# Kernel optimization log

Hardware: AMD Instinct MI355X
Metric: run time of the kernel (lower is better)

## Reference

```python
import math
import jax, jax.numpy as jnp
import numpy as np

B, T, D = 32, 2048, 512
FACTOR = 2
TOP_K = int(FACTOR * math.log(T))  # = 15, static (T is static under jit)


def setup_inputs() -> dict:
    key = jax.random.key(0)
    ks = jax.random.split(key, 11)
    s = 1.0 / math.sqrt(D)
    return {
        "query": jax.random.normal(ks[0], (B, T, D), jnp.float32),
        "key_in": jax.random.normal(ks[1], (B, T, D), jnp.float32),
        "value": jax.random.normal(ks[2], (B, T, D), jnp.float32),
        "Wq": jax.random.normal(ks[3], (D, D), jnp.float32) * s,
        "bq": jnp.zeros((D,), jnp.float32),
        "Wk": jax.random.normal(ks[4], (D, D), jnp.float32) * s,
        "bk": jnp.zeros((D,), jnp.float32),
        "Wv": jax.random.normal(ks[5], (D, D), jnp.float32) * s,
        "bv": jnp.zeros((D,), jnp.float32),
        "Wo": jax.random.normal(ks[6], (D, D), jnp.float32) * s,
        "bo": jnp.zeros((D,), jnp.float32),
    }


def reference(query, key_in, value, Wq, bq, Wk, bk, Wv, bv, Wo, bo):
    # Linear projections (query/key/value lengths are equal here, so no trimming)
    q = query @ Wq + bq      # [B, T, D]
    k = key_in @ Wk + bk     # [B, T, D]
    v = value @ Wv + bv      # [B, T, D]

    # FFT cross-correlation along the time axis
    qf = jnp.fft.rfft(q, axis=1)
    kf = jnp.fft.rfft(k, axis=1)
    attn_weights = jnp.fft.irfft(qf * jnp.conj(kf), n=T, axis=1)  # [B, T, D]

    # Top-k delay selection on the feature-mean autocorrelation
    autocorr_mean = attn_weights.mean(axis=-1)           # [B, T]
    _, topk_delays = jax.lax.top_k(autocorr_mean, TOP_K)  # [B, K] int32

    # Sum of circularly-rolled values over the top-k delays.
    # tf.roll(v, s, 0): out[t] = v[(t - s) mod T]; accumulate via scan over K
    def body(acc, d):  # d: [B] delays for this k
        rolled = jax.vmap(lambda vb, db: jnp.roll(vb, db, axis=0))(v, d)
        return acc + rolled, None

    rolled_sum, _ = jax.lax.scan(body, jnp.zeros_like(v), topk_delays.T)  # [B, T, D]

    # Softmax over the feature axis (independent of k in the original loop)
    soft_attn = jax.nn.softmax(attn_weights, axis=-1)    # [B, T, D]
    attn_output = rolled_sum * soft_attn                 # [B, T, D]

    return attn_output @ Wo + bo
```

## Files before the change

kernel.cpp:

```cpp
#include <hip/hip_runtime.h>

#define NFFT 2048
#define LDK 40
#define FFT_PAD(p) ((p) + ((p) >> 5))

typedef __attribute__((ext_vector_type(8))) short bf16x8;
typedef __attribute__((ext_vector_type(4))) float f32x4;

__device__ __forceinline__ unsigned short f2bf_rne(float x) {
  unsigned u = __float_as_uint(x);
  return (unsigned short)((u + 0x7fffu + ((u >> 16) & 1u)) >> 16);
}
__device__ __forceinline__ float bf2f(unsigned short h) {
  return __uint_as_float(((unsigned)h) << 16);
}

__device__ __forceinline__ void gemm_decode(int lin, int& n0, int& b,
                                            int& t0) {
  const int xcd = lin & 7;
  const int j = lin >> 3;
  const int nblk = j & 3;
  const int y = (j >> 2) * 8 + xcd;
  n0 = nblk * 128;
  b = y >> 4;
  t0 = (y & 15) * 128;
}

__global__ __launch_bounds__(256) void wsplit_kernel(
    const float* __restrict__ W0, const float* __restrict__ W1,
    const float* __restrict__ W2, const float* __restrict__ W3,
    unsigned short* __restrict__ out) {
  __shared__ float tile[32][33];
  const float* W = (blockIdx.z == 0) ? W0
                   : (blockIdx.z == 1) ? W1
                   : (blockIdx.z == 2) ? W2 : W3;
  unsigned short* hi = out + (size_t)blockIdx.z * 524288;
  unsigned short* lo = hi + 262144;
  const int k0 = blockIdx.x * 32, n0 = blockIdx.y * 32;
  const int c = threadIdx.x & 31, r = threadIdx.x >> 5;
#pragma unroll
  for (int p = 0; p < 4; p++)
    tile[r + 8 * p][c] = W[(size_t)(k0 + r + 8 * p) * 512 + n0 + c];
  __syncthreads();
#pragma unroll
  for (int p = 0; p < 4; p++) {
    int nn = r + 8 * p;
    float x = tile[c][nn];
    unsigned u = __float_as_uint(x);
    unsigned short h = (unsigned short)(u >> 16);
    float hf = __uint_as_float(u & 0xffff0000u);
    unsigned short l = f2bf_rne(x - hf);
    hi[(size_t)(n0 + nn) * 512 + k0 + c] = h;
    lo[(size_t)(n0 + nn) * 512 + k0 + c] = l;
  }
}

__global__ __launch_bounds__(256) void proj_gemm_split(
    const float* __restrict__ X, const unsigned short* __restrict__ WThi,
    const unsigned short* __restrict__ WTlo, const float* __restrict__ bias,
    float* __restrict__ YT) {
  __shared__ __align__(16) unsigned short Wh[128 * LDK];
  __shared__ __align__(16) unsigned short Wl[128 * LDK];
  __shared__ __align__(16) unsigned short Xh[128 * LDK];
  __shared__ __align__(16) unsigned short Xl[128 * LDK];
  const int tid = threadIdx.x;
  int n0, b, t0;
  gemm_decode(blockIdx.x, n0, b, t0);
  const int w = tid >> 6, l = tid & 63;
  const int wn = (w & 1) * 64;
  const int wt = (w >> 1) * 64;
  const int fr = l & 15;
  const int fk = (l >> 4) * 8;

  f32x4 acc[4][4];
#pragma unroll
  for (int i = 0; i < 4; i++)
#pragma unroll
    for (int j = 0; j < 4; j++) acc[i][j] = (f32x4)0.f;

  const int srow = tid >> 1, scol = (tid & 1) * 16;
  const float* Xg = X + ((size_t)(b * 2048 + t0 + srow)) * 512 + scol;
  const unsigned short* Whg = WThi + ((size_t)(n0 + srow)) * 512 + scol;
  const unsigned short* Wlg = WTlo + ((size_t)(n0 + srow)) * 512 + scol;
  unsigned short* XhL = &Xh[srow * LDK + scol];
  unsigned short* XlL = &Xl[srow * LDK + scol];
  unsigned short* WhL = &Wh[srow * LDK + scol];
  unsigned short* WlL = &Wl[srow * LDK + scol];

  float xv[16];
  uint4 wh0, wh1, wl0, wl1;
  *(float4*)&xv[0] = *(const float4*)&Xg[0];
  *(float4*)&xv[4] = *(const float4*)&Xg[4];
  *(float4*)&xv[8] = *(const float4*)&Xg[8];
  *(float4*)&xv[12] = *(const float4*)&Xg[12];
  wh0 = *(const uint4*)&Whg[0];
  wh1 = *(const uint4*)&Whg[8];
  wl0 = *(const uint4*)&Wlg[0];
  wl1 = *(const uint4*)&Wlg[8];

  for (int k0 = 0; k0 < 512; k0 += 32) {
    union { unsigned short us[16]; uint4 q[2]; } hb, lb;
#pragma unroll
    for (int i = 0; i < 16; i++) {
      unsigned u = __float_as_uint(xv[i]);
      hb.us[i] = (unsigned short)(u >> 16);
      float hf = __uint_as_float(u & 0xffff0000u);
      lb.us[i] = f2bf_rne(xv[i] - hf);
    }
    __syncthreads();
    *(uint4*)&XhL[0] = hb.q[0];
    *(uint4*)&XhL[8] = hb.q[1];
    *(uint4*)&XlL[0] = lb.q[0];
    *(uint4*)&XlL[8] = lb.q[1];
    *(uint4*)&WhL[0] = wh0;
    *(uint4*)&WhL[8] = wh1;
    *(uint4*)&WlL[0] = wl0;
    *(uint4*)&WlL[8] = wl1;
    __syncthreads();
    const int k1 = k0 + 32;
    if (k1 < 512) {
      *(float4*)&xv[0] = *(const float4*)&Xg[k1];
      *(float4*)&xv[4] = *(const float4*)&Xg[k1 + 4];
      *(float4*)&xv[8] = *(const float4*)&Xg[k1 + 8];
      *(float4*)&xv[12] = *(const float4*)&Xg[k1 + 12];
      wh0 = *(const uint4*)&Whg[k1];
      wh1 = *(const uint4*)&Whg[k1 + 8];
      wl0 = *(const uint4*)&Wlg[k1];
      wl1 = *(const uint4*)&Wlg[k1 + 8];
    }
    bf16x8 ah[4], al[4], bh[4], bl[4];
#pragma unroll
    for (int i = 0; i < 4; i++) {
      ah[i] = *(const bf16x8*)&Wh[(wn + 16 * i + fr) * LDK + fk];
      al[i] = *(const bf16x8*)&Wl[(wn + 16 * i + fr) * LDK + fk];
      bh[i] = *(const bf16x8*)&Xh[(wt + 16 * i + fr) * LDK + fk];
      bl[i] = *(const bf16x8*)&Xl[(wt + 16 * i + fr) * LDK + fk];
    }
#pragma unroll
    for (int i = 0; i < 4; i++)
#pragma unroll
      for (int j = 0; j < 4; j++) {
        acc[i][j] = __builtin_amdgcn_mfma_f32_16x16x32_bf16(ah[i], bh[j],
                                                            acc[i][j], 0, 0, 0);
        acc[i][j] = __builtin_amdgcn_mfma_f32_16x16x32_bf16(al[i], bh[j],
                                                            acc[i][j], 0, 0, 0);
        acc[i][j] = __builtin_amdgcn_mfma_f32_16x16x32_bf16(ah[i], bl[j],
                                                            acc[i][j], 0, 0, 0);
      }
  }
  const size_t obase = (size_t)b * 512 * 2048;
#pragma unroll
  for (int i = 0; i < 4; i++) {
#pragma unroll
    for (int r = 0; r < 4; r++) {
      int n = n0 + wn + 16 * i + (l >> 4) * 4 + r;
      float bsc = bias[n];
      size_t row = obase + (size_t)n * 2048 + t0 + wt + (l & 15);
#pragma unroll
      for (int j = 0; j < 4; j++) YT[row + 16 * j] = acc[i][j][r] + bsc;
    }
  }
}

__global__ __launch_bounds__(256) void gemm_bf16_vproj(
    const float* __restrict__ X, const unsigned short* __restrict__ WThi,
    const float* __restrict__ bias, unsigned short* __restrict__ Vbf) {
  __shared__ __align__(16) unsigned short Ws[128 * LDK];
  __shared__ __align__(16) unsigned short Xs[128 * LDK];
  const int tid = threadIdx.x;
  int n0, b, t0;
  gemm_decode(blockIdx.x, n0, b, t0);
  const int w = tid >> 6, l = tid & 63;
  const int wr = (w & 1) * 64;
  const int wc = (w >> 1) * 64;
  const int fr = l & 15, fk = (l >> 4) * 8;

  f32x4 acc[4][4];
#pragma unroll
  for (int i = 0; i < 4; i++)
#pragma unroll
    for (int j = 0; j < 4; j++) acc[i][j] = (f32x4)0.f;

  const int srow = tid >> 1, scol = (tid & 1) * 16;
  const float* Xg = X + ((size_t)(b * 2048 + t0 + srow)) * 512 + scol;
  const unsigned short* Wg = WThi + ((size_t)(n0 + srow)) * 512 + scol;
  unsigned short* XsL = &Xs[srow * LDK + scol];
  unsigned short* WsL = &Ws[srow * LDK + scol];

  float xv[16];
  uint4 w0, w1;
  *(float4*)&xv[0] = *(const float4*)&Xg[0];
  *(float4*)&xv[4] = *(const float4*)&Xg[4];
  *(float4*)&xv[8] = *(const float4*)&Xg[8];
  *(float4*)&xv[12] = *(const float4*)&Xg[12];
  w0 = *(const uint4*)&Wg[0];
  w1 = *(const uint4*)&Wg[8];

  for (int k0 = 0; k0 < 512; k0 += 32) {
    union { unsigned short us[16]; uint4 q[2]; } hb;
#pragma unroll
    for (int i = 0; i < 16; i++) hb.us[i] = f2bf_rne(xv[i]);
    __syncthreads();
    *(uint4*)&XsL[0] = hb.q[0];
    *(uint4*)&XsL[8] = hb.q[1];
    *(uint4*)&WsL[0] = w0;
    *(uint4*)&WsL[8] = w1;
    __syncthreads();
    const int k1 = k0 + 32;
    if (k1 < 512) {
      *(float4*)&xv[0] = *(const float4*)&Xg[k1];
      *(float4*)&xv[4] = *(const float4*)&Xg[k1 + 4];
      *(float4*)&xv[8] = *(const float4*)&Xg[k1 + 8];
      *(float4*)&xv[12] = *(const float4*)&Xg[k1 + 12];
      w0 = *(const uint4*)&Wg[k1];
      w1 = *(const uint4*)&Wg[k1 + 8];
    }
    bf16x8 af[4], bf[4];
#pragma unroll
    for (int i = 0; i < 4; i++) {
      af[i] = *(const bf16x8*)&Xs[(wr + 16 * i + fr) * LDK + fk];
      bf[i] = *(const bf16x8*)&Ws[(wc + 16 * i + fr) * LDK + fk];
    }
#pragma unroll
    for (int i = 0; i < 4; i++)
#pragma unroll
      for (int j = 0; j < 4; j++)
        acc[i][j] = __builtin_amdgcn_mfma_f32_16x16x32_bf16(af[i], bf[j],
                                                            acc[i][j], 0, 0, 0);
  }
  float bj[4];
#pragma unroll
  for (int j = 0; j < 4; j++) bj[j] = bias[n0 + wc + 16 * j + (l & 15)];
#pragma unroll
  for (int i = 0; i < 4; i++) {
#pragma unroll
    for (int r = 0; r < 4; r++) {
      int t = t0 + wr + 16 * i + (l >> 4) * 4 + r;
      unsigned short* vrow = Vbf + ((size_t)(b * 2048 + t)) * 512;
#pragma unroll
      for (int j = 0; j < 4; j++) {
        int d = n0 + wc + 16 * j + (l & 15);
        vrow[d] = f2bf_rne(acc[i][j][r] + bj[j]);
      }
    }
  }
}

__global__ __launch_bounds__(256) void gemm_bf16_out(
    const unsigned short* __restrict__ Abf,
    const unsigned short* __restrict__ WThi, const float* __restrict__ bias,
    float* __restrict__ Y) {
  __shared__ __align__(16) unsigned short Ws[128 * LDK];
  __shared__ __align__(16) unsigned short Xs[128 * LDK];
  const int tid = threadIdx.x;
  int n0, b, t0;
  gemm_decode(blockIdx.x, n0, b, t0);
  const int w = tid >> 6, l = tid & 63;
  const int wr = (w & 1) * 64;
  const int wc = (w >> 1) * 64;
  const int fr = l & 15, fk = (l >> 4) * 8;

  f32x4 acc[4][4];
#pragma unroll
  for (int i = 0; i < 4; i++)
#pragma unroll
    for (int j = 0; j < 4; j++) acc[i][j] = (f32x4)0.f;

  const int srow = tid >> 1, scol = (tid & 1) * 16;
  const unsigned short* Ag = Abf + ((size_t)(b * 2048 + t0 + srow)) * 512 + scol;
  const unsigned short* Wg = WThi + ((size_t)(n0 + srow)) * 512 + scol;
  unsigned short* XsL = &Xs[srow * LDK + scol];
  unsigned short* WsL = &Ws[srow * LDK + scol];

  uint4 a0, a1, w0, w1;
  a0 = *(const uint4*)&Ag[0];
  a1 = *(const uint4*)&Ag[8];
  w0 = *(const uint4*)&Wg[0];
  w1 = *(const uint4*)&Wg[8];

  for (int k0 = 0; k0 < 512; k0 += 32) {
    __syncthreads();
    *(uint4*)&XsL[0] = a0;
    *(uint4*)&XsL[8] = a1;
    *(uint4*)&WsL[0] = w0;
    *(uint4*)&WsL[8] = w1;
    __syncthreads();
    const int k1 = k0 + 32;
    if (k1 < 512) {
      a0 = *(const uint4*)&Ag[k1];
      a1 = *(const uint4*)&Ag[k1 + 8];
      w0 = *(const uint4*)&Wg[k1];
      w1 = *(const uint4*)&Wg[k1 + 8];
    }
    bf16x8 af[4], bf[4];
#pragma unroll
    for (int i = 0; i < 4; i++) {
      af[i] = *(const bf16x8*)&Xs[(wr + 16 * i + fr) * LDK + fk];
      bf[i] = *(const bf16x8*)&Ws[(wc + 16 * i + fr) * LDK + fk];
    }
#pragma unroll
    for (int i = 0; i < 4; i++)
#pragma unroll
      for (int j = 0; j < 4; j++)
        acc[i][j] = __builtin_amdgcn_mfma_f32_16x16x32_bf16(af[i], bf[j],
                                                            acc[i][j], 0, 0, 0);
  }
  float bj[4];
#pragma unroll
  for (int j = 0; j < 4; j++) bj[j] = bias[n0 + wc + 16 * j + (l & 15)];
#pragma unroll
  for (int i = 0; i < 4; i++) {
#pragma unroll
    for (int r = 0; r < 4; r++) {
      int t = t0 + wr + 16 * i + (l >> 4) * 4 + r;
      float* yrow = Y + ((size_t)(b * 2048 + t)) * 512;
#pragma unroll
      for (int j = 0; j < 4; j++) {
        int n = n0 + wc + 16 * j + (l & 15);
        yrow[n] = acc[i][j][r] + bj[j];
      }
    }
  }
}

__device__ __forceinline__ float2 cadd(float2 a, float2 b) {
  return make_float2(a.x + b.x, a.y + b.y);
}
__device__ __forceinline__ float2 csub(float2 a, float2 b) {
  return make_float2(a.x - b.x, a.y - b.y);
}
__device__ __forceinline__ float2 cmulf(float2 a, float2 b) {
  return make_float2(a.x * b.x - a.y * b.y, a.x * b.y + a.y * b.x);
}
template <int SGN>
__device__ __forceinline__ float2 mul_i(float2 a) {
  return (SGN < 0) ? make_float2(a.y, -a.x) : make_float2(-a.y, a.x);
}

template <int SGN>
__device__ __forceinline__ void dft4(float2 v[4]) {
  float2 b0 = cadd(v[0], v[2]);
  float2 b2 = csub(v[0], v[2]);
  float2 b1 = cadd(v[1], v[3]);
  float2 b3 = mul_i<SGN>(csub(v[1], v[3]));
  v[0] = cadd(b0, b1);
  v[2] = csub(b0, b1);
  v[1] = cadd(b2, b3);
  v[3] = csub(b2, b3);
}

template <int SGN>
__device__ __forceinline__ void dft8(float2 v[8]) {
  const float C = 0.70710678118654752f;
  float2 e[4], o[4];
#pragma unroll
  for (int i = 0; i < 4; i++) {
    e[i] = cadd(v[i], v[i + 4]);
    o[i] = csub(v[i], v[i + 4]);
  }
  {
    float s = o[1].x, t = o[1].y;
    o[1] = (SGN < 0) ? make_float2(C * (s + t), C * (t - s))
                     : make_float2(C * (s - t), C * (s + t));
  }
  o[2] = mul_i<SGN>(o[2]);
  {
    float s = o[3].x, t = o[3].y;
    o[3] = (SGN < 0) ? make_float2(C * (t - s), -C * (s + t))
                     : make_float2(-C * (s + t), C * (s - t));
  }
  dft4<SGN>(e);
  dft4<SGN>(o);
  v[0] = e[0]; v[2] = e[1]; v[4] = e[2]; v[6] = e[3];
  v[1] = o[0]; v[3] = o[1]; v[5] = o[2]; v[7] = o[3];
}

__device__ __forceinline__ void twiddle8_pair(float2 vz[8], float2 vw[8],
                                              float ang) {
  float2 T;
  __sincosf(ang, &T.y, &T.x);
  float2 t = T;
  vz[1] = cmulf(vz[1], t);
  vw[1] = cmulf(vw[1], t);
#pragma unroll
  for (int r = 2; r < 8; r++) {
    t = cmulf(t, T);
    vz[r] = cmulf(vz[r], t);
    vw[r] = cmulf(vw[r], t);
  }
}
__device__ __forceinline__ void twiddle8_one(float2 v[8], float ang) {
  float2 T;
  __sincosf(ang, &T.y, &T.x);
  float2 t = T;
  v[1] = cmulf(v[1], t);
#pragma unroll
  for (int r = 2; r < 8; r++) {
    t = cmulf(t, T);
    v[r] = cmulf(v[r], t);
  }
}

__global__ __launch_bounds__(256) void fft_correlate(
    float* __restrict__ qT, const float* __restrict__ kT) {
  __shared__ float2 ldsZ[2112];
  __shared__ float2 ldsW[2112];
  const int b = blockIdx.x;
  const int d0 = blockIdx.y * 2;
  const int tid = threadIdx.x;
  const size_t base = ((size_t)b * 512 + d0) * 2048;

  const float W1 = -6.28318530717958647692f / 2048.f;
  const int j2 = tid & 31, j3 = tid & 3;
  const int s1 = tid >> 5, s2 = tid >> 2;
  const int f1 = ((tid & 7) << 6) | (tid & 56) | (tid >> 6);
  const int pt = tid + (tid >> 5);
  const int b2 = 264 * s1 + j2;
  const int b3 = 33 * s2 + j3;

  float2 vz[8], vw[8];
#pragma unroll
  for (int r = 0; r < 8; r++) {
    int t = tid + (r << 8);
    vz[r] = make_float2(qT[base + t], qT[base + 2048 + t]);
    vw[r] = make_float2(kT[base + t], kT[base + 2048 + t]);
  }

  dft8<-1>(vz);
  dft8<-1>(vw);
  twiddle8_pair(vz, vw, W1 * (float)tid);
#pragma unroll
  for (int r = 0; r < 8; r++) {
    ldsZ[pt + 264 * r] = vz[r];
    ldsW[pt + 264 * r] = vw[r];
  }
  __syncthreads();
#pragma unroll
  for (int m = 0; m < 8; m++) {
    vz[m] = ldsZ[b2 + 33 * m];
    vw[m] = ldsW[b2 + 33 * m];
  }
  dft8<-1>(vz);
  dft8<-1>(vw);
  twiddle8_pair(vz, vw, (W1 * 8.f) * (float)j2);
#pragma unroll
  for (int r = 0; r < 8; r++) {
    ldsZ[b2 + 33 * r] = vz[r];
    ldsW[b2 + 33 * r] = vw[r];
  }
  __syncthreads();
#pragma unroll
  for (int m = 0; m < 8; m++) {
    vz[m] = ldsZ[b3 + 4 * m];
    vw[m] = ldsW[b3 + 4 * m];
  }
  dft8<-1>(vz);
  dft8<-1>(vw);
  twiddle8_pair(vz, vw, (W1 * 64.f) * (float)j3);
#pragma unroll
  for (int r = 0; r < 8; r++) {
    ldsZ[b3 + 4 * r] = vz[r];
    ldsW[b3 + 4 * r] = vw[r];
  }
  __syncthreads();
  {
    float2 za[4], zb[4], wa[4], wb[4];
    const int pb = f1 << 2;
#pragma unroll
    for (int c = 0; c < 4; c++) {
      za[c] = ldsZ[FFT_PAD(pb + c)];
      zb[c] = ldsZ[FFT_PAD(pb + 16 + c)];
      wa[c] = ldsW[FFT_PAD(pb + c)];
      wb[c] = ldsW[FFT_PAD(pb + 16 + c)];
    }
    dft4<-1>(za);
    dft4<-1>(zb);
    dft4<-1>(wa);
    dft4<-1>(wb);
    __syncthreads();
#pragma unroll
    for (int c = 0; c < 4; c++) {
      ldsZ[pt + 528 * c] = za[c];
      ldsZ[pt + 264 + 528 * c] = zb[c];
      ldsW[pt + 528 * c] = wa[c];
      ldsW[pt + 264 + 528 * c] = wb[c];
    }
  }
  __syncthreads();

  float2 G[8];
#pragma unroll
  for (int r = 0; r < 8; r++) {
    int f = tid + (r << 8);
    int fn = (NFFT - f) & (NFFT - 1);
    float2 Zf = ldsZ[pt + 264 * r], Zn = ldsZ[FFT_PAD(fn)];
    float2 Wf = ldsW[pt + 264 * r], Wn = ldsW[FFT_PAD(fn)];
    float A1x = Zf.x + Zn.x, A1y = Zf.y - Zn.y;
    float B1x = Wf.x + Wn.x, B1y = Wn.y - Wf.y;
    float A2x = Zf.x - Zn.x, A2y = Zf.y + Zn.y;
    float B2x = Wf.x - Wn.x, B2y = -Wf.y - Wn.y;
    float p1x = A1x * B1x - A1y * B1y;
    float p1y = A1x * B1y + A1y * B1x;
    float p2x = A2x * B2x - A2y * B2y;
    float p2y = A2x * B2y + A2y * B2x;
    G[r] = make_float2(0.25f * (p1x - p2y), 0.25f * (p1y + p2x));
    (void)f;
  }
  __syncthreads();

  dft8<1>(G);
  twiddle8_one(G, (-W1) * (float)tid);
#pragma unroll
  for (int r = 0; r < 8; r++) ldsZ[pt + 264 * r] = G[r];
  __syncthreads();
#pragma unroll
  for (int m = 0; m < 8; m++) G[m] = ldsZ[b2 + 33 * m];
  dft8<1>(G);
  twiddle8_one(G, (-W1 * 8.f) * (float)j2);
#pragma unroll
  for (int r = 0; r < 8; r++) ldsZ[b2 + 33 * r] = G[r];
  __syncthreads();
#pragma unroll
  for (int m = 0; m < 8; m++) G[m] = ldsZ[b3 + 4 * m];
  dft8<1>(G);
  twiddle8_one(G, (-W1 * 64.f) * (float)j3);
#pragma unroll
  for (int r = 0; r < 8; r++) ldsZ[b3 + 4 * r] = G[r];
  __syncthreads();
  {
    float2 za[4], zb[4];
    const int pb = f1 << 2;
#pragma unroll
    for (int c = 0; c < 4; c++) {
      za[c] = ldsZ[FFT_PAD(pb + c)];
      zb[c] = ldsZ[FFT_PAD(pb + 16 + c)];
    }
    dft4<1>(za);
    dft4<1>(zb);
    const float scale = 1.0f / (float)NFFT;
#pragma unroll
    for (int c = 0; c < 4; c++) {
      int ta = tid + (c << 9);
      int tb = ta + 256;
      qT[base + ta] = za[c].x * scale;
      qT[base + 2048 + ta] = za[c].y * scale;
      qT[base + tb] = zb[c].x * scale;
      qT[base + 2048 + tb] = zb[c].y * scale;
    }
  }
}

__global__ __launch_bounds__(256) void colstats_kernel(
    const float* __restrict__ attnT, float* __restrict__ mean,
    float2* __restrict__ stats) {
  const int b = blockIdx.x;
  const int t = blockIdx.y * 256 + threadIdx.x;
  const size_t base = (size_t)b * 512 * 2048 + t;
  float sum = 0.f, m = -1e30f, s = 0.f;
  for (int d = 0; d < 512; d++) {
    float a = attnT[base + (size_t)d * 2048];
    sum += a;
    float mn = fmaxf(m, a);
    s = s * __expf(m - mn) + __expf(a - mn);
    m = mn;
  }
  mean[b * 2048 + t] = sum * (1.f / 512.f);
  stats[b * 2048 + t] = make_float2(m, s);
}

__global__ __launch_bounds__(256) void topk_kernel(
    const float* __restrict__ mean, int* __restrict__ delays) {
  __shared__ float vals[2048];
  __shared__ float sv[256];
  __shared__ int si[256];
  const int b = blockIdx.x, tid = threadIdx.x;
#pragma unroll
  for (int r = 0; r < 8; r++)
    vals[tid + (r << 8)] = mean[b * 2048 + tid + (r << 8)];
  __syncthreads();
  for (int k = 0; k < 15; k++) {
    float bv = -1e30f;
    int bi = 1 << 30;
#pragma unroll
    for (int r = 0; r < 8; r++) {
      int i = (r << 8) + tid;
      float v = vals[i];
      if (v > bv || (v == bv && i < bi)) { bv = v; bi = i; }
    }
    sv[tid] = bv;
    si[tid] = bi;
    __syncthreads();
    for (int off = 128; off > 0; off >>= 1) {
      if (tid < off) {
        float v2 = sv[tid + off];
        int i2 = si[tid + off];
        if (v2 > sv[tid] || (v2 == sv[tid] && i2 < si[tid])) {
          sv[tid] = v2;
          si[tid] = i2;
        }
      }
      __syncthreads();
    }
    if (tid == 0) {
      delays[b * 15 + k] = si[0];
      vals[si[0]] = -1e30f;
    }
    __syncthreads();
  }
}

__global__ __launch_bounds__(256) void ctx_kernel(
    const float* __restrict__ attnT, const unsigned short* __restrict__ vbf,
    const float2* __restrict__ stats, const int* __restrict__ delays,
    unsigned short* __restrict__ ctx) {
  __shared__ float atile[64][65];
  __shared__ int dly[15];
  const int lin = blockIdx.x;
  const int g = lin >> 8;
  const int r = lin & 255;
  const int b = g * 8 + (r & 7);
  const int tb = (r >> 3) * 64;
  const int tid = threadIdx.x;
  if (tid < 15) dly[tid] = delays[b * 15 + tid];
  __syncthreads();

  const int tl = tid >> 2;
  const int dq = (tid & 3) * 16;
  const int tq = (tid & 3) * 4;
  const int t = tb + tl;
  const float2 st = stats[b * 2048 + t];
  const float m = st.x, inv_s = 1.f / st.y;

  int rowoff[15];
#pragma unroll
  for (int k = 0; k < 15; k++)
    rowoff[k] = ((t - dly[k]) & 2047) * 512;

  const size_t vbase = (size_t)b * 2048 * 512;
  const size_t abase = (size_t)b * 512 * 2048;

  for (int d0 = 0; d0 < 512; d0 += 64) {
    __syncthreads();
#pragma unroll
    for (int tt = 0; tt < 4; tt++) {
      float4 a4 = *(const float4*)&attnT[abase + (size_t)(d0 + tl) * 2048 +
                                         tb + tt * 16 + tq];
      atile[tt * 16 + tq + 0][tl] = a4.x;
      atile[tt * 16 + tq + 1][tl] = a4.y;
      atile[tt * 16 + tq + 2][tl] = a4.z;
      atile[tt * 16 + tq + 3][tl] = a4.w;
    }
    __syncthreads();

    float rolled[16];
#pragma unroll
    for (int i = 0; i < 16; i++) rolled[i] = 0.f;
#pragma unroll
    for (int k = 0; k < 15; k++) {
      const uint4* vp = (const uint4*)(vbf + vbase + rowoff[k] + d0 + dq);
      uint4 v0 = vp[0], v1 = vp[1];
      unsigned uu[8] = {v0.x, v0.y, v0.z, v0.w, v1.x, v1.y, v1.z, v1.w};
#pragma unroll
      for (int w = 0; w < 8; w++) {
        rolled[2 * w + 0] += __uint_as_float(uu[w] << 16);
        rolled[2 * w + 1] += __uint_as_float(uu[w] & 0xffff0000u);
      }
    }

    union { unsigned short us[16]; uint4 q[2]; } ob;
#pragma unroll
    for (int i = 0; i < 16; i++) {
      float a = atile[tl][dq + i];
      float p = __expf(a - m) * inv_s;
      ob.us[i] = f2bf_rne(p * rolled[i]);
    }
    uint4* op = (uint4*)(ctx + vbase + (size_t)t * 512 + d0 + dq);
    op[0] = ob.q[0];
    op[1] = ob.q[1];
  }
}

extern "C" void kernel_launch(void* const* d_in, const int* in_sizes, int n_in,
                              void* d_out, int out_size, void* d_ws,
                              size_t ws_size, hipStream_t stream) {
  const float* query = (const float*)d_in[0];
  const float* key_in = (const float*)d_in[1];
  const float* value = (const float*)d_in[2];
  const float* Wq = (const float*)d_in[3];
  const float* bq = (const float*)d_in[4];
  const float* Wk = (const float*)d_in[5];
  const float* bk = (const float*)d_in[6];
  const float* Wv = (const float*)d_in[7];
  const float* bv = (const float*)d_in[8];
  const float* Wo = (const float*)d_in[9];
  const float* bo = (const float*)d_in[10];
  float* out = (float*)d_out;

  float* ws = (float*)d_ws;
  const size_t SZ = (size_t)32 * 512 * 2048;
  float* qT = ws;
  float* kT = ws + SZ;
  unsigned short* vbf = (unsigned short*)(ws + SZ);
  unsigned short* ctxbf = (unsigned short*)(ws + SZ + SZ / 2);
  unsigned short* wbuf = (unsigned short*)(ws + 2 * SZ);
  float* mean = ws + 2 * SZ + 1048576;
  float2* stats = (float2*)(ws + 2 * SZ + 1048576 + 65536);
  int* delays = (int*)(ws + 2 * SZ + 1048576 + 65536 + 131072);

  const unsigned short* wq_hi = wbuf + 0 * 524288;
  const unsigned short* wq_lo = wq_hi + 262144;
  const unsigned short* wk_hi = wbuf + 1 * 524288;
  const unsigned short* wk_lo = wk_hi + 262144;
  const unsigned short* wv_hi = wbuf + 2 * 524288;
  const unsigned short* wo_hi = wbuf + 3 * 524288;

  wsplit_kernel<<<dim3(16, 16, 4), 256, 0, stream>>>(Wq, Wk, Wv, Wo, wbuf);

  proj_gemm_split<<<2048, 256, 0, stream>>>(query, wq_hi, wq_lo, bq, qT);
  proj_gemm_split<<<2048, 256, 0, stream>>>(key_in, wk_hi, wk_lo, bk, kT);

  fft_correlate<<<dim3(32, 256), 256, 0, stream>>>(qT, kT);

  gemm_bf16_vproj<<<2048, 256, 0, stream>>>(value, wv_hi, bv, vbf);

  colstats_kernel<<<dim3(32, 8), 256, 0, stream>>>(qT, mean, stats);
  topk_kernel<<<32, 256, 0, stream>>>(mean, delays);
  ctx_kernel<<<1024, 256, 0, stream>>>(qT, vbf, stats, delays, ctxbf);

  gemm_bf16_out<<<2048, 256, 0, stream>>>(ctxbf, wo_hi, bo, out);
}
```

Before: 984.5 us.

## Stream GEMM tiles into LDS via direct global-to-LDS loads with double buffering

The weight-split kernel now writes the transposed weights in a tiled, XOR-swizzled layout, one 128x32 block per K-step. The three GEMM kernels fetch those tiles, and in the output GEMM also the bf16 activations, straight into double-buffered LDS with global_load_lds. This removes the register round trip and one of the two barriers per K-step. The goal is to overlap the next tile's fetch with the current MFMAs and avoid LDS bank conflicts without padding. The catch is that correctness now depends on the compiler placing vmcnt waits before the barrier for the asynchronous LDS writes, and LDS use goes up.

```diff
diff --git a/kernel.cpp b/kernel.cpp
--- a/kernel.cpp
+++ b/kernel.cpp
@@ -13,6 +13,13 @@
 }
 __device__ __forceinline__ float bf2f(unsigned short h) {
   return __uint_as_float(((unsigned)h) << 16);
+}
+
+__device__ __forceinline__ void gload_lds16(const unsigned short* g,
+                                            unsigned short* l) {
+  __builtin_amdgcn_global_load_lds(
+      (__attribute__((address_space(1))) void*)(g),
+      (__attribute__((address_space(3))) void*)(l), 16, 0, 0);
 }
 
 __device__ __forceinline__ void gemm_decode(int lin, int& n0, int& b,
@@ -42,16 +49,22 @@
   for (int p = 0; p < 4; p++)
     tile[r + 8 * p][c] = W[(size_t)(k0 + r + 8 * p) * 512 + n0 + c];
   __syncthreads();
+  const int kt = k0 >> 5;
+  const int cc = c >> 3, s = c & 7;
 #pragma unroll
   for (int p = 0; p < 4; p++) {
     int nn = r + 8 * p;
+    int n = n0 + nn;
     float x = tile[c][nn];
     unsigned u = __float_as_uint(x);
     unsigned short h = (unsigned short)(u >> 16);
     float hf = __uint_as_float(u & 0xffff0000u);
     unsigned short l = f2bf_rne(x - hf);
-    hi[(size_t)(n0 + nn) * 512 + k0 + c] = h;
-    lo[(size_t)(n0 + nn) * 512 + k0 + c] = l;
+    int nt = n >> 7, rr = n & 127;
+    int swz = cc ^ ((rr >> 1) & 3);
+    size_t off = (size_t)(nt * 16 + kt) * 4096 + rr * 32 + swz * 8 + s;
+    hi[off] = h;
+    lo[off] = l;
   }
 }
 
@@ -59,18 +72,20 @@
     const float* __restrict__ X, const unsigned short* __restrict__ WThi,
     const unsigned short* __restrict__ WTlo, const float* __restrict__ bias,
     float* __restrict__ YT) {
-  __shared__ __align__(16) unsigned short Wh[128 * LDK];
-  __shared__ __align__(16) unsigned short Wl[128 * LDK];
+  __shared__ __align__(16) unsigned short Wh[2][4096];
+  __shared__ __align__(16) unsigned short Wl[2][4096];
   __shared__ __align__(16) unsigned short Xh[128 * LDK];
   __shared__ __align__(16) unsigned short Xl[128 * LDK];
   const int tid = threadIdx.x;
   int n0, b, t0;
   gemm_decode(blockIdx.x, n0, b, t0);
-  const int w = tid >> 6, l = tid & 63;
-  const int wn = (w & 1) * 64;
-  const int wt = (w >> 1) * 64;
+  const int wv = tid >> 6, l = tid & 63;
+  const int wn = (wv & 1) * 64;
+  const int wt = (wv >> 1) * 64;
   const int fr = l & 15;
-  const int fk = (l >> 4) * 8;
+  const int fj = l >> 4;
+  const int fk = fj * 8;
+  const int wchunk = (fj ^ ((fr >> 1) & 3)) * 8;
 
   f32x4 acc[4][4];
 #pragma unroll
@@ -80,25 +95,32 @@
 
   const int srow = tid >> 1, scol = (tid & 1) * 16;
   const float* Xg = X + ((size_t)(b * 2048 + t0 + srow)) * 512 + scol;
-  const unsigned short* Whg = WThi + ((size_t)(n0 + srow)) * 512 + scol;
-  const unsigned short* Wlg = WTlo + ((size_t)(n0 + srow)) * 512 + scol;
   unsigned short* XhL = &Xh[srow * LDK + scol];
   unsigned short* XlL = &Xl[srow * LDK + scol];
-  unsigned short* WhL = &Wh[srow * LDK + scol];
-  unsigned short* WlL = &Wl[srow * LDK + scol];
+
+  const unsigned short* WhT =
+      WThi + (size_t)(n0 >> 7) * 65536 + wv * 1024 + l * 8;
+  const unsigned short* WlT =
+      WTlo + (size_t)(n0 >> 7) * 65536 + wv * 1024 + l * 8;
+
+  auto dma_w = [&](int ktile, int buf) {
+    const unsigned short* sh = WhT + (size_t)ktile * 4096;
+    const unsigned short* sl = WlT + (size_t)ktile * 4096;
+    gload_lds16(sh, &Wh[buf][wv * 1024]);
+    gload_lds16(sh + 512, &Wh[buf][wv * 1024 + 512]);
+    gload_lds16(sl, &Wl[buf][wv * 1024]);
+    gload_lds16(sl + 512, &Wl[buf][wv * 1024 + 512]);
+  };
 
   float xv[16];
-  uint4 wh0, wh1, wl0, wl1;
   *(float4*)&xv[0] = *(const float4*)&Xg[0];
   *(float4*)&xv[4] = *(const float4*)&Xg[4];
   *(float4*)&xv[8] = *(const float4*)&Xg[8];
   *(float4*)&xv[12] = *(const float4*)&Xg[12];
-  wh0 = *(const uint4*)&Whg[0];
-  wh1 = *(const uint4*)&Whg[8];
-  wl0 = *(const uint4*)&Wlg[0];
-  wl1 = *(const uint4*)&Wlg[8];
-
-  for (int k0 = 0; k0 < 512; k0 += 32) {
+  dma_w(0, 0);
+  int cur = 0;
+
+  for (int ks = 0; ks < 16; ks++) {
     union { unsigned short us[16]; uint4 q[2]; } hb, lb;
 #pragma unroll
     for (int i = 0; i < 16; i++) {
@@ -112,27 +134,20 @@
     *(uint4*)&XhL[8] = hb.q[1];
     *(uint4*)&XlL[0] = lb.q[0];
     *(uint4*)&XlL[8] = lb.q[1];
-    *(uint4*)&WhL[0] = wh0;
-    *(uint4*)&WhL[8] = wh1;
-    *(uint4*)&WlL[0] = wl0;
-    *(uint4*)&WlL[8] = wl1;
-    __syncthreads();
-    const int k1 = k0 + 32;
-    if (k1 < 512) {
+    __syncthreads();
+    if (ks < 15) {
+      const int k1 = ks * 32 + 32;
       *(float4*)&xv[0] = *(const float4*)&Xg[k1];
       *(float4*)&xv[4] = *(const float4*)&Xg[k1 + 4];
       *(float4*)&xv[8] = *(const float4*)&Xg[k1 + 8];
       *(float4*)&xv[12] = *(const float4*)&Xg[k1 + 12];
-      wh0 = *(const uint4*)&Whg[k1];
-      wh1 = *(const uint4*)&Whg[k1 + 8];
-      wl0 = *(const uint4*)&Wlg[k1];
-      wl1 = *(const uint4*)&Wlg[k1 + 8];
+      dma_w(ks + 1, cur ^ 1);
     }
     bf16x8 ah[4], al[4], bh[4], bl[4];
 #pragma unroll
     for (int i = 0; i < 4; i++) {
-      ah[i] = *(const bf16x8*)&Wh[(wn + 16 * i + fr) * LDK + fk];
-      al[i] = *(const bf16x8*)&Wl[(wn + 16 * i + fr) * LDK + fk];
+      ah[i] = *(const bf16x8*)&Wh[cur][(wn + 16 * i + fr) * 32 + wchunk];
+      al[i] = *(const bf16x8*)&Wl[cur][(wn + 16 * i + fr) * 32 + wchunk];
       bh[i] = *(const bf16x8*)&Xh[(wt + 16 * i + fr) * LDK + fk];
       bl[i] = *(const bf16x8*)&Xl[(wt + 16 * i + fr) * LDK + fk];
     }
@@ -147,6 +162,7 @@
         acc[i][j] = __builtin_amdgcn_mfma_f32_16x16x32_bf16(ah[i], bl[j],
                                                             acc[i][j], 0, 0, 0);
       }
+    cur ^= 1;
   }
   const size_t obase = (size_t)b * 512 * 2048;
 #pragma unroll
@@ -165,15 +181,16 @@
 __global__ __launch_bounds__(256) void gemm_bf16_vproj(
     const float* __restrict__ X, const unsigned short* __restrict__ WThi,
     const float* __restrict__ bias, unsigned short* __restrict__ Vbf) {
-  __shared__ __align__(16) unsigned short Ws[128 * LDK];
+  __shared__ __align__(16) unsigned short Ws[2][4096];
   __shared__ __align__(16) unsigned short Xs[128 * LDK];
   const int tid = threadIdx.x;
   int n0, b, t0;
   gemm_decode(blockIdx.x, n0, b, t0);
-  const int w = tid >> 6, l = tid & 63;
-  const int wr = (w & 1) * 64;
-  const int wc = (w >> 1) * 64;
-  const int fr = l & 15, fk = (l >> 4) * 8;
+  const int wv = tid >> 6, l = tid & 63;
+  const int wr = (wv & 1) * 64;
+  const int wc = (wv >> 1) * 64;
+  const int fr = l & 15, fj = l >> 4, fk = fj * 8;
+  const int wchunk = (fj ^ ((fr >> 1) & 3)) * 8;
 
   f32x4 acc[4][4];
 #pragma unroll
@@ -183,43 +200,45 @@
 
   const int srow = tid >> 1, scol = (tid & 1) * 16;
   const float* Xg = X + ((size_t)(b * 2048 + t0 + srow)) * 512 + scol;
-  const unsigned short* Wg = WThi + ((size_t)(n0 + srow)) * 512 + scol;
   unsigned short* XsL = &Xs[srow * LDK + scol];
-  unsigned short* WsL = &Ws[srow * LDK + scol];
+
+  const unsigned short* WT =
+      WThi + (size_t)(n0 >> 7) * 65536 + wv * 1024 + l * 8;
+  auto dma_w = [&](int ktile, int buf) {
+    const unsigned short* s = WT + (size_t)ktile * 4096;
+    gload_lds16(s, &Ws[buf][wv * 1024]);
+    gload_lds16(s + 512, &Ws[buf][wv * 1024 + 512]);
+  };
 
   float xv[16];
-  uint4 w0, w1;
   *(float4*)&xv[0] = *(const float4*)&Xg[0];
   *(float4*)&xv[4] = *(const float4*)&Xg[4];
   *(float4*)&xv[8] = *(const float4*)&Xg[8];
   *(float4*)&xv[12] = *(const float4*)&Xg[12];
-  w0 = *(const uint4*)&Wg[0];
-  w1 = *(const uint4*)&Wg[8];
-
-  for (int k0 = 0; k0 < 512; k0 += 32) {
+  dma_w(0, 0);
+  int cur = 0;
+
+  for (int ks = 0; ks < 16; ks++) {
     union { unsigned short us[16]; uint4 q[2]; } hb;
 #pragma unroll
     for (int i = 0; i < 16; i++) hb.us[i] = f2bf_rne(xv[i]);
     __syncthreads();
     *(uint4*)&XsL[0] = hb.q[0];
     *(uint4*)&XsL[8] = hb.q[1];
-    *(uint4*)&WsL[0] = w0;
-    *(uint4*)&WsL[8] = w1;
-    __syncthreads();
-    const int k1 = k0 + 32;
-    if (k1 < 512) {
+    __syncthreads();
+    if (ks < 15) {
+      const int k1 = ks * 32 + 32;
       *(float4*)&xv[0] = *(const float4*)&Xg[k1];
       *(float4*)&xv[4] = *(const float4*)&Xg[k1 + 4];
       *(float4*)&xv[8] = *(const float4*)&Xg[k1 + 8];
       *(float4*)&xv[12] = *(const float4*)&Xg[k1 + 12];
-      w0 = *(const uint4*)&Wg[k1];
-      w1 = *(const uint4*)&Wg[k1 + 8];
+      dma_w(ks + 1, cur ^ 1);
     }
     bf16x8 af[4], bf[4];
 #pragma unroll
     for (int i = 0; i < 4; i++) {
       af[i] = *(const bf16x8*)&Xs[(wr + 16 * i + fr) * LDK + fk];
-      bf[i] = *(const bf16x8*)&Ws[(wc + 16 * i + fr) * LDK + fk];
+      bf[i] = *(const bf16x8*)&Ws[cur][(wc + 16 * i + fr) * 32 + wchunk];
     }
 #pragma unroll
     for (int i = 0; i < 4; i++)
@@ -227,6 +246,7 @@
       for (int j = 0; j < 4; j++)
         acc[i][j] = __builtin_amdgcn_mfma_f32_16x16x32_bf16(af[i], bf[j],
                                                             acc[i][j], 0, 0, 0);
+    cur ^= 1;
   }
   float bj[4];
 #pragma unroll
@@ -248,17 +268,18 @@
 
 __global__ __launch_bounds__(256) void gemm_bf16_out(
     const unsigned short* __restrict__ Abf,
-    const unsigned short* __restrict__ WThi, const float* __restrict__ bias,
+    const unsigned short* __restrict__ WT, const float* __restrict__ bias,
     float* __restrict__ Y) {
-  __shared__ __align__(16) unsigned short Ws[128 * LDK];
-  __shared__ __align__(16) unsigned short Xs[128 * LDK];
+  __shared__ __align__(16) unsigned short As[2][4096];
+  __shared__ __align__(16) unsigned short Ws[2][4096];
   const int tid = threadIdx.x;
   int n0, b, t0;
   gemm_decode(blockIdx.x, n0, b, t0);
-  const int w = tid >> 6, l = tid & 63;
-  const int wr = (w & 1) * 64;
-  const int wc = (w >> 1) * 64;
-  const int fr = l & 15, fk = (l >> 4) * 8;
+  const int wv = tid >> 6, l = tid & 63;
+  const int wr = (wv & 1) * 64;
+  const int wc = (wv >> 1) * 64;
+  const int fr = l & 15, fj = l >> 4;
+  const int wchunk = (fj ^ ((fr >> 1) & 3)) * 8;
 
   f32x4 acc[4][4];
 #pragma unroll
@@ -266,37 +287,33 @@
 #pragma unroll
     for (int j = 0; j < 4; j++) acc[i][j] = (f32x4)0.f;
 
-  const int srow = tid >> 1, scol = (tid & 1) * 16;
-  const unsigned short* Ag = Abf + ((size_t)(b * 2048 + t0 + srow)) * 512 + scol;
-  const unsigned short* Wg = WThi + ((size_t)(n0 + srow)) * 512 + scol;
-  unsigned short* XsL = &Xs[srow * LDK + scol];
-  unsigned short* WsL = &Ws[srow * LDK + scol];
-
-  uint4 a0, a1, w0, w1;
-  a0 = *(const uint4*)&Ag[0];
-  a1 = *(const uint4*)&Ag[8];
-  w0 = *(const uint4*)&Wg[0];
-  w1 = *(const uint4*)&Wg[8];
-
-  for (int k0 = 0; k0 < 512; k0 += 32) {
-    __syncthreads();
-    *(uint4*)&XsL[0] = a0;
-    *(uint4*)&XsL[8] = a1;
-    *(uint4*)&WsL[0] = w0;
-    *(uint4*)&WsL[8] = w1;
-    __syncthreads();
-    const int k1 = k0 + 32;
-    if (k1 < 512) {
-      a0 = *(const uint4*)&Ag[k1];
-      a1 = *(const uint4*)&Ag[k1 + 8];
-      w0 = *(const uint4*)&Wg[k1];
-      w1 = *(const uint4*)&Wg[k1 + 8];
-    }
+  const unsigned short* WTb =
+      WT + (size_t)(n0 >> 7) * 65536 + wv * 1024 + l * 8;
+  const int arow = wv * 32 + (l >> 2);
+  const int ac = (l & 3) ^ ((arow >> 1) & 3);
+  const unsigned short* Ab1 =
+      Abf + ((size_t)(b * 2048 + t0 + arow)) * 512 + ac * 8;
+  const unsigned short* Ab2 =
+      Abf + ((size_t)(b * 2048 + t0 + arow + 16)) * 512 + ac * 8;
+
+  auto dma = [&](int ks, int buf) {
+    const unsigned short* w = WTb + (size_t)ks * 4096;
+    gload_lds16(w, &Ws[buf][wv * 1024]);
+    gload_lds16(w + 512, &Ws[buf][wv * 1024 + 512]);
+    gload_lds16(Ab1 + ks * 32, &As[buf][wv * 1024]);
+    gload_lds16(Ab2 + ks * 32, &As[buf][wv * 1024 + 512]);
+  };
+
+  dma(0, 0);
+  int cur = 0;
+  for (int ks = 0; ks < 16; ks++) {
+    __syncthreads();
+    if (ks < 15) dma(ks + 1, cur ^ 1);
     bf16x8 af[4], bf[4];
 #pragma unroll
     for (int i = 0; i < 4; i++) {
-      af[i] = *(const bf16x8*)&Xs[(wr + 16 * i + fr) * LDK + fk];
-      bf[i] = *(const bf16x8*)&Ws[(wc + 16 * i + fr) * LDK + fk];
+      af[i] = *(const bf16x8*)&As[cur][(wr + 16 * i + fr) * 32 + wchunk];
+      bf[i] = *(const bf16x8*)&Ws[cur][(wc + 16 * i + fr) * 32 + wchunk];
     }
 #pragma unroll
     for (int i = 0; i < 4; i++)
@@ -304,6 +321,7 @@
       for (int j = 0; j < 4; j++)
         acc[i][j] = __builtin_amdgcn_mfma_f32_16x16x32_bf16(af[i], bf[j],
                                                             acc[i][j], 0, 0, 0);
+    cur ^= 1;
   }
   float bj[4];
 #pragma unroll
```

Result: slower. 1.051 ms (+6.8%).
